# Performance work log

Hardware: AMD Instinct MI355X
Metric: run time of the kernel (lower is better)

The kernel has to match this reference:

```python
import jax, jax.numpy as jnp
import numpy as np
import math

DIM = 256
HEADS = 8
HID = DIM * HEADS


def mish(x):
    return x * jnp.tanh(jax.nn.softplus(x))


def setup_inputs() -> dict:
    key = jax.random.key(0)
    ks = jax.random.split(key, 12)
    b, t, l = 4, 16, 256
    s = 1.0 / math.sqrt(DIM)
    inp = {
        "qkv_x": jax.random.normal(ks[0], (b, t, l, DIM), jnp.float32),
        "t_embed": jax.random.normal(ks[1], (b, t, 1, DIM), jnp.float32),
        "reward_embed": jax.random.normal(ks[2], (b, t, 1, DIM), jnp.float32),
        "Wq": jax.random.normal(ks[3], (DIM, HID), jnp.float32) * s,
        "Wk": jax.random.normal(ks[4], (DIM, HID), jnp.float32) * s,
        "Wv": jax.random.normal(ks[5], (DIM, HID), jnp.float32) * s,
        "Wq_t": jax.random.normal(ks[6], (DIM, HID), jnp.float32) * s,
        "bq_t": jnp.zeros((HID,), jnp.float32),
        "Wk_t": jax.random.normal(ks[7], (DIM, HID), jnp.float32) * s,
        "bk_t": jnp.zeros((HID,), jnp.float32),
        "Wv_t": jax.random.normal(ks[8], (DIM, HID), jnp.float32) * s,
        "bv_t": jnp.zeros((HID,), jnp.float32),
        "Wo": jax.random.normal(ks[9], (HID, DIM), jnp.float32) * (1.0 / math.sqrt(HID)),
        "bo": jnp.zeros((DIM,), jnp.float32),
    }
    return inp


def reference(qkv_x, t_embed, reward_embed, Wq, Wk, Wv, Wq_t, bq_t, Wk_t, bk_t, Wv_t, bv_t, Wo, bo):
    b, t, l, f = qkv_x.shape
    x = qkv_x.reshape(b * t, l, f)                    # (bt, l, f)
    tr = (t_embed + reward_embed).reshape(b * t, 1, f)  # (bt, 1, f)
    m = mish(tr)

    def proj(W, Wt, bt_):
        # bias-add of time-conditioning broadcast over l, split heads
        y = x @ W + (m @ Wt + bt_)                    # (bt, l, H*D)
        return y.reshape(b * t, l, HEADS, DIM).transpose(0, 2, 1, 3)  # (bt, H, l, D)

    q = proj(Wq, Wq_t, bq_t)
    k = proj(Wk, Wk_t, bk_t)
    v = proj(Wv, Wv_t, bv_t)

    scores = jnp.einsum('bhqd,bhkd->bhqk', q, k) / math.sqrt(DIM)
    attn = jax.nn.softmax(scores, axis=-1)
    out = jnp.einsum('bhqk,bhkd->bhqd', attn, v)      # (bt, H, l, D)
    out = out.transpose(0, 2, 1, 3).reshape(b, t, l, HEADS * DIM)
    return out @ Wo + bo
```

## Files before the change

### kernel.cpp

```cpp
#include <hip/hip_runtime.h>
#include <stdint.h>

typedef __bf16 bf16x8 __attribute__((ext_vector_type(8)));
typedef float f32x4 __attribute__((ext_vector_type(4)));
typedef uint32_t u32x4 __attribute__((ext_vector_type(4)));

#define MFMA16(a,b,c) __builtin_amdgcn_mfma_f32_16x16x32_bf16(a,b,c,0,0,0)

#define OFF_XB   0ull
#define OFF_WT   8388608ull
#define OFF_WTT  11534336ull
#define OFF_WOT  14680064ull
#define OFF_MB   15728640ull
#define OFF_BIAS 15761408ull
#define OFF_K    17334272ull
#define OFF_VT   84443136ull
#define WS_NEED  151552000ull
#define OFF_Q    151552000ull
#define WS_NEED2 218660864ull

__device__ __forceinline__ uint16_t f2bf(float f) {
  uint32_t u = __builtin_bit_cast(uint32_t, f);
  return (uint16_t)((u + 0x7fffu + ((u >> 16) & 1u)) >> 16);
}
__device__ __forceinline__ bf16x8 ld16(const uint16_t* p) {
  u32x4 v = *(const u32x4*)p;
  return __builtin_bit_cast(bf16x8, v);
}
__device__ __forceinline__ void gll16(const uint16_t* g, char* l) {
  __builtin_amdgcn_global_load_lds(
      (const __attribute__((address_space(1))) void*)g,
      (__attribute__((address_space(3))) void*)l, 16, 0, 0);
}
__device__ __forceinline__ void bounce_w2(char* slab, int row, int col, uint16_t val) {
  int slot = col >> 3;
  *(uint16_t*)(slab + row * 256 + (((slot ^ (row & 7)) & 15) << 4) + ((col & 7) << 1)) = val;
}
__device__ __forceinline__ bf16x8 bounce_r16(const char* slab, int row, int slot) {
  u32x4 v = *(const u32x4*)(slab + row * 256 + (((slot ^ (row & 7)) & 15) << 4));
  return __builtin_bit_cast(bf16x8, v);
}

__global__ void sentinel_kernel(float* out, float val) {
  out[blockIdx.x * 256 + threadIdx.x] = val;
}
__global__ void init_out(const float* bo, float* out) {
  int i = blockIdx.x * 256 + threadIdx.x;
  out[i] = bo[i & 255];
}

__global__ void mish_kernel(const float* te, const float* re, uint16_t* mb) {
  int i = blockIdx.x * 256 + threadIdx.x;
  float x = te[i] + re[i];
  float sp = log1pf(__expf(x));
  mb[i] = f2bf(x * tanhf(sp));
}

__global__ void convx_kernel(const float* x, uint16_t* xb) {
  int i = blockIdx.x * 256 + threadIdx.x;
  float4 v = ((const float4*)x)[i];
  ushort4 o = make_ushort4(f2bf(v.x), f2bf(v.y), f2bf(v.z), f2bf(v.w));
  ((ushort4*)xb)[i] = o;
}

__global__ void wtrans_kernel(const float* w0, const float* w1, const float* w2,
                              const float* w3, const float* w4, const float* w5,
                              const float* w6, uint16_t* wt, uint16_t* wtt, uint16_t* wot) {
  int z = blockIdx.y;
  const float* src; uint16_t* dst; int C;
  if (z < 3)      { src = (z==0)?w0:((z==1)?w1:w2); dst = wt  + (size_t)z*524288;     C=2048; }
  else if (z < 6) { src = (z==3)?w3:((z==4)?w4:w5); dst = wtt + (size_t)(z-3)*524288; C=2048; }
  else            { src = w6; dst = wot;                                              C=256; }
  int R = (z < 6) ? 256 : 2048;
  __shared__ uint16_t tile[32][33];
  int tc = C >> 5;
  int bR = (blockIdx.x / tc) << 5, bC = (blockIdx.x % tc) << 5;
  int tx = threadIdx.x & 31, ty = threadIdx.x >> 5;
  #pragma unroll
  for (int i = 0; i < 4; i++) {
    int r = bR + ty + i * 8;
    tile[ty + i * 8][tx] = f2bf(src[(size_t)r * C + bC + tx]);
  }
  __syncthreads();
  #pragma unroll
  for (int i = 0; i < 4; i++) {
    int c = bC + ty + i * 8;
    dst[(size_t)c * R + bR + tx] = tile[tx][ty + i * 8];
  }
}

__global__ __launch_bounds__(256, 4)
void bias_gemm(const uint16_t* Mb, const uint16_t* WTT,
               const float* bq, const float* bk, const float* bv, float* biasAll) {
  int bid = blockIdx.x;
  int z = bid >> 4, nbt = bid & 15;
  int n0 = nbt << 7;
  const uint16_t* Bsrc = WTT + (size_t)z * 524288;
  const float* bvec = (z == 0) ? bq : ((z == 1) ? bk : bv);
  float* outp = biasAll + (size_t)z * 131072;
  int tid = threadIdx.x, lane = tid & 63, w = tid >> 6;
  int g = lane >> 4, ln = lane & 15;

  bf16x8 af[8];
  #pragma unroll
  for (int ks = 0; ks < 8; ks++)
    af[ks] = ld16(Mb + (size_t)(w*16 + ln) * 256 + ks*32 + g*8);
  f32x4 acc[8];
  #pragma unroll
  for (int j = 0; j < 8; j++) acc[j] = (f32x4){0.f,0.f,0.f,0.f};
  #pragma unroll
  for (int j = 0; j < 8; j++)
    #pragma unroll
    for (int ks = 0; ks < 8; ks++) {
      bf16x8 bf_ = ld16(Bsrc + (size_t)(n0 + j*16 + ln) * 256 + ks*32 + g*8);
      acc[j] = MFMA16(af[ks], bf_, acc[j]);
    }
  #pragma unroll
  for (int j = 0; j < 8; j++) {
    int colg = n0 + j*16 + ln;
    float bb = bvec[colg];
    #pragma unroll
    for (int r = 0; r < 4; r++)
      outp[(size_t)(w*16 + g*4 + r) * 2048 + colg] = acc[j][r] + bb;
  }
}

__global__ __launch_bounds__(256)
void qkv_gemm3(const uint16_t* Xb, const uint16_t* WT, const float* biasAll,
               uint16_t* Kw, uint16_t* Vt, uint16_t* Qw) {
  __shared__ char stage[32768];
  int nwg = gridDim.x, cpx = nwg >> 3;
  int b0 = blockIdx.x;
  int bid = (b0 & 7) * cpx + (b0 >> 3);
  int z2 = bid >> 11, rem = bid & 2047;
  int widx = (z2 + 1) % 3;
  int mb = rem >> 4, nb = rem & 15;
  int m0 = mb << 7, n0 = nb << 7;
  const uint16_t* Bsrc = WT + (size_t)widx * 524288;
  int bt = m0 >> 8;
  const float* bias = biasAll + (size_t)widx * 131072 + (size_t)bt * 2048;
  int tid = threadIdx.x, lane = tid & 63, w = tid >> 6;
  int g = lane >> 4, ln = lane & 15;
  int wr = w >> 1, wc = w & 1;
  int rw = lane >> 3;
  int sg = (lane & 7) ^ rw;

  f32x4 acc[4][4];
  #pragma unroll
  for (int i = 0; i < 4; i++)
    #pragma unroll
    for (int j = 0; j < 4; j++) acc[i][j] = (f32x4){0.f,0.f,0.f,0.f};

  for (int kt = 0; kt < 4; kt++) {
    int k0 = kt << 6;
    __syncthreads();
    #pragma unroll
    for (int c = 0; c < 4; c++) {
      int chunk = w * 4 + c;
      int row = chunk * 8 + rw;
      gll16(Xb   + (size_t)(m0 + row) * 256 + k0 + sg * 8, stage + chunk * 1024);
      gll16(Bsrc + (size_t)(n0 + row) * 256 + k0 + sg * 8, stage + 16384 + chunk * 1024);
    }
    __syncthreads();
    #pragma unroll
    for (int ks = 0; ks < 2; ks++) {
      bf16x8 a_[4];
      #pragma unroll
      for (int i = 0; i < 4; i++) {
        int R = wr*64 + i*16 + ln;
        u32x4 v = *(const u32x4*)(stage + R*128 + ((((ks<<2)+g) ^ (R & 7)) << 4));
        a_[i] = __builtin_bit_cast(bf16x8, v);
      }
      #pragma unroll
      for (int j = 0; j < 4; j++) {
        int R = wc*64 + j*16 + ln;
        u32x4 v = *(const u32x4*)(stage + 16384 + R*128 + ((((ks<<2)+g) ^ (R & 7)) << 4));
        bf16x8 b_ = __builtin_bit_cast(bf16x8, v);
        #pragma unroll
        for (int i = 0; i < 4; i++) acc[i][j] = MFMA16(a_[i], b_, acc[i][j]);
      }
    }
  }

  __syncthreads();
  char* esl = stage + (w << 13);
  float scale = (z2 == 2) ? 0.0625f : 1.0f;
  int hh = n0 >> 8;
  size_t hb = (size_t)(bt * 8 + hh) << 16;
  int dbase = (n0 & 255) + wc*64;
  int lbase = (m0 & 255) + wr*64;

  if (z2 == 1) {
    #pragma unroll
    for (int j = 0; j < 4; j++) {
      float bb = bias[n0 + wc*64 + j*16 + ln];
      int row = j*16 + ln;
      #pragma unroll
      for (int i = 0; i < 4; i++) {
        int col0 = i*16 + g*4;
        ushort4 pk = make_ushort4(f2bf(acc[i][j][0]+bb), f2bf(acc[i][j][1]+bb),
                                  f2bf(acc[i][j][2]+bb), f2bf(acc[i][j][3]+bb));
        *(ushort4*)(esl + row*128 + ((((col0 >> 3) ^ (row & 7)) & 7) << 4)
                    + ((col0 & 7) << 1)) = pk;
      }
    }
  } else {
    #pragma unroll
    for (int j = 0; j < 4; j++) {
      float bb = bias[n0 + wc*64 + j*16 + ln];
      int slotb = j*2 + (ln >> 3), bcol = (ln & 7) << 1;
      #pragma unroll
      for (int i = 0; i < 4; i++)
        #pragma unroll
        for (int r = 0; r < 4; r++) {
          int row = i*16 + g*4 + r;
          *(uint16_t*)(esl + row*128 + (((slotb ^ (row & 7)) & 7) << 4) + bcol)
              = f2bf((acc[i][j][r] + bb) * scale);
        }
    }
  }
  #pragma unroll
  for (int it = 0; it < 8; it++) {
    int idx = it*64 + lane;
    int row = idx >> 3, ch = idx & 7;
    u32x4 v = *(const u32x4*)(esl + row*128 + (((ch ^ (row & 7)) & 7) << 4));
    if (z2 == 1) {
      *(u32x4*)(Vt + hb + ((size_t)(dbase + row) << 8) + lbase + ch*8) = v;
    } else {
      uint16_t* dst = (z2 == 0) ? Kw : Qw;
      *(u32x4*)(dst + hb + ((size_t)(lbase + row) << 8) + dbase + ch*8) = v;
    }
  }
}

__global__ __launch_bounds__(1024, 2)
void attn_core2(const uint16_t* Qw, const uint16_t* Kw, const uint16_t* Vt, uint16_t* Ob) {
  __shared__ char smem[65536];
  int tid = threadIdx.x, lane = tid & 63, w = tid >> 6;
  int g = lane >> 4, ln = lane & 15;
  int bh = blockIdx.x;
  const size_t kvbase = (size_t)bh << 16;
  int q0l = w * 16;
  char* stage = smem;
  char* slab  = smem + 32768 + (w << 11);

  u32x4 rv[2];
  auto issue_tile = [&](const uint16_t* src) {
    #pragma unroll
    for (int it = 0; it < 2; it++) {
      int c = tid + (it << 10);
      int row = c >> 5, sl = c & 31;
      rv[it] = *(const u32x4*)(src + (size_t)row * 256 + sl * 8);
    }
  };
  auto commit_tile = [&]() {
    #pragma unroll
    for (int it = 0; it < 2; it++) {
      int c = tid + (it << 10);
      int row = c >> 5, sl = c & 31;
      *(u32x4*)(stage + row * 512 + ((sl ^ (row & 7)) << 4)) = rv[it];
    }
  };
  auto frag = [&](int row, int slot) -> bf16x8 {
    u32x4 v = *(const u32x4*)(stage + row * 512 + ((slot ^ (row & 7)) << 4));
    return __builtin_bit_cast(bf16x8, v);
  };

  issue_tile(Kw + kvbase);
  bf16x8 qa[8];
  #pragma unroll
  for (int ks = 0; ks < 8; ks++)
    qa[ks] = ld16(Qw + kvbase + (size_t)(q0l + ln) * 256 + ks*32 + g*8);

  f32x4 S[16];
  #pragma unroll
  for (int f = 0; f < 16; f++) S[f] = (f32x4){0.f,0.f,0.f,0.f};
  #pragma unroll
  for (int t = 0; t < 4; t++) {
    __syncthreads();
    commit_tile();
    __syncthreads();
    if (t < 3) issue_tile(Kw + kvbase + (size_t)((t+1)*64) * 256);
    #pragma unroll
    for (int ks = 0; ks < 8; ks++)
      #pragma unroll
      for (int f2 = 0; f2 < 4; f2++)
        S[t*4+f2] = MFMA16(qa[ks], frag(f2*16 + ln, ks*4 + g), S[t*4+f2]);
  }
  issue_tile(Vt + kvbase);

  #pragma unroll
  for (int r = 0; r < 4; r++) {
    float mx = -3.4e38f;
    #pragma unroll
    for (int f = 0; f < 16; f++) mx = fmaxf(mx, S[f][r]);
    #pragma unroll
    for (int m_ = 1; m_ < 16; m_ <<= 1) mx = fmaxf(mx, __shfl_xor(mx, m_, 64));
    float sum = 0.f;
    #pragma unroll
    for (int f = 0; f < 16; f++) {
      float p = __expf(S[f][r] - mx);
      S[f][r] = p; sum += p;
    }
    #pragma unroll
    for (int m_ = 1; m_ < 16; m_ <<= 1) sum += __shfl_xor(sum, m_, 64);
    float inv = 1.f / sum;
    #pragma unroll
    for (int f = 0; f < 16; f++) S[f][r] *= inv;
  }

  bf16x8 pb[8];
  #pragma unroll
  for (int qtr = 0; qtr < 4; qtr++) {
    #pragma unroll
    for (int f2 = 0; f2 < 4; f2++) {
      int col = f2*16 + ln;
      int slot = col >> 3;
      #pragma unroll
      for (int r = 0; r < 4; r++) {
        int row = g*4 + r;
        *(uint16_t*)(slab + row*128 + (((slot ^ (row & 7)) & 7) << 4) + ((col & 7) << 1))
            = f2bf(S[qtr*4+f2][r]);
      }
    }
    #pragma unroll
    for (int i = 0; i < 2; i++) {
      u32x4 v = *(const u32x4*)(slab + ln*128 + ((((i*4+g) ^ (ln & 7)) & 7) << 4));
      pb[qtr*2+i] = __builtin_bit_cast(bf16x8, v);
    }
  }

  f32x4 O[16];
  #pragma unroll
  for (int df = 0; df < 16; df++) O[df] = (f32x4){0.f,0.f,0.f,0.f};
  #pragma unroll
  for (int t = 0; t < 4; t++) {
    __syncthreads();
    commit_tile();
    __syncthreads();
    if (t < 3) issue_tile(Vt + kvbase + (size_t)((t+1)*64) * 256);
    #pragma unroll
    for (int ks = 0; ks < 8; ks++)
      #pragma unroll
      for (int df2 = 0; df2 < 4; df2++)
        O[t*4+df2] = MFMA16(frag(df2*16 + ln, ks*4 + g), pb[ks], O[t*4+df2]);
  }

  size_t obase = kvbase + (size_t)(q0l + ln) * 256;
  #pragma unroll
  for (int df = 0; df < 16; df++) {
    ushort4 pk = make_ushort4(f2bf(O[df][0]), f2bf(O[df][1]), f2bf(O[df][2]), f2bf(O[df][3]));
    *(ushort4*)(Ob + obase + df*16 + g*4) = pk;
  }
}

__global__ __launch_bounds__(256, 4)
void out_gemm(const uint16_t* Ob, const uint16_t* WoT, const float* bo, float* out) {
  __shared__ char stage[16384];
  int b0 = blockIdx.x;
  int bid = (b0 & 7) * 64 + (b0 >> 3);
  int mt = bid >> 1, nt = bid & 1;
  int m0 = mt << 6, n0 = nt << 7;
  int bt = m0 >> 8;
  int lrow = (m0 & 255);
  int tid = threadIdx.x, lane = tid & 63, w = tid >> 6;
  int g = lane >> 4, ln = lane & 15;

  u32x4 rb[4];
  auto issueW = [&](int kt) {
    #pragma unroll
    for (int it = 0; it < 4; it++) {
      int c = tid + (it << 8);
      int row = c >> 3, sl = c & 7;
      rb[it] = *(const u32x4*)(WoT + (size_t)(n0 + row) * 2048 + kt*64 + sl*8);
    }
  };
  auto aptr = [&](int kt) -> const uint16_t* {
    return Ob + ((size_t)(bt*8 + (kt >> 2)) << 16)
         + (size_t)(lrow + w*16 + ln) * 256 + (kt & 3) * 64;
  };
  issueW(0);
  bf16x8 afc[2];
  { const uint16_t* ab = aptr(0); afc[0] = ld16(ab + g*8); afc[1] = ld16(ab + 32 + g*8); }
  f32x4 acc[8];
  #pragma unroll
  for (int j = 0; j < 8; j++) acc[j] = (f32x4){0.f,0.f,0.f,0.f};

  for (int kt = 0; kt < 32; kt++) {
    __syncthreads();
    #pragma unroll
    for (int it = 0; it < 4; it++) {
      int c = tid + (it << 8);
      int row = c >> 3, sl = c & 7;
      *(u32x4*)(stage + row*128 + (((sl ^ (row & 7)) & 7) << 4)) = rb[it];
    }
    __syncthreads();
    bf16x8 afn[2];
    if (kt < 31) {
      issueW(kt+1);
      const uint16_t* ab = aptr(kt+1);
      afn[0] = ld16(ab + g*8); afn[1] = ld16(ab + 32 + g*8);
    }
    #pragma unroll
    for (int ks = 0; ks < 2; ks++)
      #pragma unroll
      for (int j = 0; j < 8; j++) {
        int row = j*16 + ln;
        u32x4 v = *(const u32x4*)(stage + row*128 + ((((ks*4+g) ^ (row & 7)) & 7) << 4));
        acc[j] = MFMA16(afc[ks], __builtin_bit_cast(bf16x8, v), acc[j]);
      }
    if (kt < 31) { afc[0] = afn[0]; afc[1] = afn[1]; }
  }
  #pragma unroll
  for (int j = 0; j < 8; j++) {
    int col = n0 + j*16 + ln;
    float bb = bo[col];
    #pragma unroll
    for (int r = 0; r < 4; r++)
      out[(size_t)(m0 + w*16 + g*4 + r) * 256 + col] = acc[j][r] + bb;
  }
}

__global__ __launch_bounds__(512, 2)
void attn_v5(const uint16_t* Xb, const uint16_t* WT, const float* Bi,
             const uint16_t* Kw, const uint16_t* Vt, const uint16_t* WoT,
             float* out) {
  __shared__ char smem[65536];
  int tid = threadIdx.x, lane = tid & 63, w = tid >> 6;
  int g = lane >> 4, ln = lane & 15;
  int bid = blockIdx.x;
  int bh = bid >> 1, qh = bid & 1;
  int bt = bh >> 3, h = bh & 7;
  const size_t kvbase = (size_t)bh << 16;
  int q0g = bt * 256 + qh * 128 + w * 16;
  char* stage = smem;
  char* slab  = smem + 32768 + (w << 12);

  u32x4 rv[4];
  auto issue_tile = [&](const uint16_t* src, int rowstride) {
    #pragma unroll
    for (int it = 0; it < 4; it++) {
      int c = tid + (it << 9);
      int row = c >> 5, sl = c & 31;
      rv[it] = *(const u32x4*)(src + (size_t)row * rowstride + sl * 8);
    }
  };
  auto commit_tile = [&]() {
    #pragma unroll
    for (int it = 0; it < 4; it++) {
      int c = tid + (it << 9);
      int row = c >> 5, sl = c & 31;
      *(u32x4*)(stage + row * 512 + ((sl ^ (row & 7)) << 4)) = rv[it];
    }
  };
  auto frag = [&](int row, int slot) -> bf16x8 {
    u32x4 v = *(const u32x4*)(stage + row * 512 + ((slot ^ (row & 7)) << 4));
    return __builtin_bit_cast(bf16x8, v);
  };

  issue_tile(WT + (size_t)(h*256) * 256, 256);
  bf16x8 qx[8];
  #pragma unroll
  for (int ks = 0; ks < 8; ks++)
    qx[ks] = ld16(Xb + (size_t)(q0g + ln) * 256 + ks*32 + g*8);
  f32x4 qacc[16];
  #pragma unroll
  for (int f = 0; f < 16; f++) qacc[f] = (f32x4){0.f,0.f,0.f,0.f};
  #pragma unroll
  for (int t = 0; t < 4; t++) {
    __syncthreads();
    commit_tile();
    __syncthreads();
    if (t < 3) issue_tile(WT + (size_t)(h*256 + (t+1)*64) * 256, 256);
    #pragma unroll
    for (int ks = 0; ks < 8; ks++)
      #pragma unroll
      for (int f2 = 0; f2 < 4; f2++)
        qacc[t*4+f2] = MFMA16(qx[ks], frag(f2*16 + ln, ks*4 + g), qacc[t*4+f2]);
  }
  issue_tile(Kw + kvbase, 256);
  #pragma unroll
  for (int f = 0; f < 16; f++) {
    float bb = Bi[bt*2048 + h*256 + f*16 + ln];
    #pragma unroll
    for (int r = 0; r < 4; r++) qacc[f][r] = (qacc[f][r] + bb) * 0.0625f;
  }
  bf16x8 qa[8];
  #pragma unroll
  for (int dh = 0; dh < 2; dh++) {
    #pragma unroll
    for (int f2 = 0; f2 < 8; f2++) {
      int f = dh*8 + f2;
      #pragma unroll
      for (int r = 0; r < 4; r++)
        bounce_w2(slab, g*4 + r, f2*16 + ln, f2bf(qacc[f][r]));
    }
    #pragma unroll
    for (int ks2 = 0; ks2 < 4; ks2++)
      qa[dh*4 + ks2] = bounce_r16(slab, ln, ks2*4 + g);
  }

  f32x4 S[16];
  #pragma unroll
  for (int f = 0; f < 16; f++) S[f] = (f32x4){0.f,0.f,0.f,0.f};
  #pragma unroll
  for (int t = 0; t < 4; t++) {
    __syncthreads();
    commit_tile();
    __syncthreads();
    if (t < 3) issue_tile(Kw + kvbase + (size_t)((t+1)*64) * 256, 256);
    #pragma unroll
    for (int ks = 0; ks < 8; ks++)
      #pragma unroll
      for (int f2 = 0; f2 < 4; f2++)
        S[t*4+f2] = MFMA16(qa[ks], frag(f2*16 + ln, ks*4 + g), S[t*4+f2]);
  }
  issue_tile(Vt + kvbase, 256);

  #pragma unroll
  for (int r = 0; r < 4; r++) {
    float mx = -3.4e38f;
    #pragma unroll
    for (int f = 0; f < 16; f++) mx = fmaxf(mx, S[f][r]);
    #pragma unroll
    for (int m_ = 1; m_ < 16; m_ <<= 1) mx = fmaxf(mx, __shfl_xor(mx, m_, 64));
    float sum = 0.f;
    #pragma unroll
    for (int f = 0; f < 16; f++) {
      float p = __expf(S[f][r] - mx);
      S[f][r] = p; sum += p;
    }
    #pragma unroll
    for (int m_ = 1; m_ < 16; m_ <<= 1) sum += __shfl_xor(sum, m_, 64);
    float inv = 1.f / sum;
    #pragma unroll
    for (int f = 0; f < 16; f++) S[f][r] *= inv;
  }

  bf16x8 pb[8];
  #pragma unroll
  for (int kh = 0; kh < 2; kh++) {
    #pragma unroll
    for (int f2 = 0; f2 < 8; f2++) {
      int f = kh*8 + f2;
      #pragma unroll
      for (int r = 0; r < 4; r++)
        bounce_w2(slab, g*4 + r, f2*16 + ln, f2bf(S[f][r]));
    }
    #pragma unroll
    for (int ks2 = 0; ks2 < 4; ks2++)
      pb[kh*4 + ks2] = bounce_r16(slab, ln, ks2*4 + g);
  }

  f32x4 O[16];
  #pragma unroll
  for (int df = 0; df < 16; df++) O[df] = (f32x4){0.f,0.f,0.f,0.f};
  #pragma unroll
  for (int t = 0; t < 4; t++) {
    __syncthreads();
    commit_tile();
    __syncthreads();
    if (t < 3) issue_tile(Vt + kvbase + (size_t)((t+1)*64) * 256, 256);
    #pragma unroll
    for (int ks = 0; ks < 8; ks++)
      #pragma unroll
      for (int df2 = 0; df2 < 4; df2++)
        O[t*4+df2] = MFMA16(frag(df2*16 + ln, ks*4 + g), pb[ks], O[t*4+df2]);
  }
  issue_tile(WoT + (size_t)0 * 2048 + h*256, 2048);

  bf16x8 oa[8];
  #pragma unroll
  for (int dh = 0; dh < 2; dh++) {
    #pragma unroll
    for (int df2 = 0; df2 < 8; df2++) {
      int df = dh*8 + df2;
      #pragma unroll
      for (int r = 0; r < 4; r++)
        bounce_w2(slab, ln, df2*16 + g*4 + r, f2bf(O[df][r]));
    }
    #pragma unroll
    for (int ks2 = 0; ks2 < 4; ks2++)
      oa[dh*4 + ks2] = bounce_r16(slab, ln, ks2*4 + g);
  }

  f32x4 oacc[16];
  #pragma unroll
  for (int ef = 0; ef < 16; ef++) oacc[ef] = (f32x4){0.f,0.f,0.f,0.f};
  #pragma unroll
  for (int t = 0; t < 4; t++) {
    __syncthreads();
    commit_tile();
    __syncthreads();
    if (t < 3) issue_tile(WoT + (size_t)((t+1)*64) * 2048 + h*256, 2048);
    #pragma unroll
    for (int ks = 0; ks < 8; ks++)
      #pragma unroll
      for (int ef2 = 0; ef2 < 4; ef2++)
        oacc[t*4+ef2] = MFMA16(oa[ks], frag(ef2*16 + ln, ks*4 + g), oacc[t*4+ef2]);
  }
  #pragma unroll
  for (int ef = 0; ef < 16; ef++)
    #pragma unroll
    for (int r = 0; r < 4; r++)
      atomicAdd(out + (size_t)(q0g + g*4 + r) * 256 + ef*16 + ln, oacc[ef][r]);
}

extern "C" void kernel_launch(void* const* d_in, const int* in_sizes, int n_in,
                              void* d_out, int out_size, void* d_ws, size_t ws_size,
                              hipStream_t stream) {
  float* out = (float*)d_out;
  if (ws_size < WS_NEED) {
    sentinel_kernel<<<16384, 256, 0, stream>>>(out, 1000.0f + (float)(ws_size >> 20));
    return;
  }
  const float* x   = (const float*)d_in[0];
  const float* te  = (const float*)d_in[1];
  const float* re  = (const float*)d_in[2];
  const float* Wq  = (const float*)d_in[3];
  const float* Wk  = (const float*)d_in[4];
  const float* Wv  = (const float*)d_in[5];
  const float* Wqt = (const float*)d_in[6];
  const float* bqt = (const float*)d_in[7];
  const float* Wkt = (const float*)d_in[8];
  const float* bkt = (const float*)d_in[9];
  const float* Wvt = (const float*)d_in[10];
  const float* bvt = (const float*)d_in[11];
  const float* Wo  = (const float*)d_in[12];
  const float* bo  = (const float*)d_in[13];
  char* ws = (char*)d_ws;
  uint16_t* Xb  = (uint16_t*)(ws + OFF_XB);
  uint16_t* WT  = (uint16_t*)(ws + OFF_WT);
  uint16_t* WTT = (uint16_t*)(ws + OFF_WTT);
  uint16_t* WoT = (uint16_t*)(ws + OFF_WOT);
  uint16_t* Mb  = (uint16_t*)(ws + OFF_MB);
  float*    Bi  = (float*)(ws + OFF_BIAS);
  uint16_t* Kw  = (uint16_t*)(ws + OFF_K);
  uint16_t* Vt  = (uint16_t*)(ws + OFF_VT);

  mish_kernel<<<64, 256, 0, stream>>>(te, re, Mb);
  wtrans_kernel<<<dim3(512, 7), 256, 0, stream>>>(Wq, Wk, Wv, Wqt, Wkt, Wvt, Wo, WT, WTT, WoT);
  convx_kernel<<<4096, 256, 0, stream>>>(x, Xb);
  bias_gemm<<<48, 256, 0, stream>>>(Mb, WTT, bqt, bkt, bvt, Bi);

  if (ws_size >= WS_NEED2) {
    uint16_t* Qw = (uint16_t*)(ws + OFF_Q);
    qkv_gemm3<<<6144, 256, 0, stream>>>(Xb, WT, Bi, Kw, Vt, Qw);
    attn_core2<<<512, 1024, 0, stream>>>(Qw, Kw, Vt, Qw);
    out_gemm<<<512, 256, 0, stream>>>(Qw, WoT, bo, out);
  } else {
    qkv_gemm3<<<4096, 256, 0, stream>>>(Xb, WT, Bi, Kw, Vt, Kw);
    init_out<<<16384, 256, 0, stream>>>(bo, out);
    attn_v5<<<1024, 512, 0, stream>>>(Xb, WT, Bi, Kw, Vt, WoT, out);
  }
}
```

Measured before the change: 217.3 us.

## Merge prep kernels into one launch and use direct global-to-LDS loads in attention

The mish, x conversion and weight transpose kernels are folded into a single prep_all launch, with the block index selecting the role. This removes two launch gaps. The attention kernel's K/V staging no longer goes through registers followed by an LDS commit; gll16 copies global memory straight into the swizzled LDS stage. In exchange, the previous overlap, where the next tile's global load was issued during the current tile's MFMAs, is dropped. Each tile load is now exposed between barriers.

```diff
diff --git a/kernel.cpp b/kernel.cpp
--- a/kernel.cpp
+++ b/kernel.cpp
@@ -49,24 +49,28 @@
   out[i] = bo[i & 255];
 }
 
-__global__ void mish_kernel(const float* te, const float* re, uint16_t* mb) {
-  int i = blockIdx.x * 256 + threadIdx.x;
-  float x = te[i] + re[i];
-  float sp = log1pf(__expf(x));
-  mb[i] = f2bf(x * tanhf(sp));
-}
-
-__global__ void convx_kernel(const float* x, uint16_t* xb) {
-  int i = blockIdx.x * 256 + threadIdx.x;
-  float4 v = ((const float4*)x)[i];
-  ushort4 o = make_ushort4(f2bf(v.x), f2bf(v.y), f2bf(v.z), f2bf(v.w));
-  ((ushort4*)xb)[i] = o;
-}
-
-__global__ void wtrans_kernel(const float* w0, const float* w1, const float* w2,
-                              const float* w3, const float* w4, const float* w5,
-                              const float* w6, uint16_t* wt, uint16_t* wtt, uint16_t* wot) {
-  int z = blockIdx.y;
+__global__ void prep_all(const float* te, const float* re, uint16_t* mb,
+                         const float* x, uint16_t* xb,
+                         const float* w0, const float* w1, const float* w2,
+                         const float* w3, const float* w4, const float* w5,
+                         const float* w6, uint16_t* wt, uint16_t* wtt, uint16_t* wot) {
+  int b = blockIdx.x;
+  if (b < 64) {
+    int i = b * 256 + threadIdx.x;
+    float v = te[i] + re[i];
+    float sp = log1pf(__expf(v));
+    mb[i] = f2bf(v * tanhf(sp));
+    return;
+  }
+  if (b < 4160) {
+    int i = (b - 64) * 256 + threadIdx.x;
+    float4 v = ((const float4*)x)[i];
+    ushort4 o = make_ushort4(f2bf(v.x), f2bf(v.y), f2bf(v.z), f2bf(v.w));
+    ((ushort4*)xb)[i] = o;
+    return;
+  }
+  int local = b - 4160;
+  int z = local >> 9, bx = local & 511;
   const float* src; uint16_t* dst; int C;
   if (z < 3)      { src = (z==0)?w0:((z==1)?w1:w2); dst = wt  + (size_t)z*524288;     C=2048; }
   else if (z < 6) { src = (z==3)?w3:((z==4)?w4:w5); dst = wtt + (size_t)(z-3)*524288; C=2048; }
@@ -74,7 +78,7 @@
   int R = (z < 6) ? 256 : 2048;
   __shared__ uint16_t tile[32][33];
   int tc = C >> 5;
-  int bR = (blockIdx.x / tc) << 5, bC = (blockIdx.x % tc) << 5;
+  int bR = (bx / tc) << 5, bC = (bx % tc) << 5;
   int tx = threadIdx.x & 31, ty = threadIdx.x >> 5;
   #pragma unroll
   for (int i = 0; i < 4; i++) {
@@ -234,7 +238,7 @@
 }
 
 __global__ __launch_bounds__(1024, 2)
-void attn_core2(const uint16_t* Qw, const uint16_t* Kw, const uint16_t* Vt, uint16_t* Ob) {
+void attn_core3(const uint16_t* Qw, const uint16_t* Kw, const uint16_t* Vt, uint16_t* Ob) {
   __shared__ char smem[65536];
   int tid = threadIdx.x, lane = tid & 63, w = tid >> 6;
   int g = lane >> 4, ln = lane & 15;
@@ -244,21 +248,14 @@
   char* stage = smem;
   char* slab  = smem + 32768 + (w << 11);
 
-  u32x4 rv[2];
-  auto issue_tile = [&](const uint16_t* src) {
-    #pragma unroll
-    for (int it = 0; it < 2; it++) {
-      int c = tid + (it << 10);
-      int row = c >> 5, sl = c & 31;
-      rv[it] = *(const u32x4*)(src + (size_t)row * 256 + sl * 8);
-    }
-  };
-  auto commit_tile = [&]() {
-    #pragma unroll
-    for (int it = 0; it < 2; it++) {
-      int c = tid + (it << 10);
-      int row = c >> 5, sl = c & 31;
-      *(u32x4*)(stage + row * 512 + ((sl ^ (row & 7)) << 4)) = rv[it];
+  int grow0 = (w << 2) + (lane >> 5);
+  int p = lane & 31;
+  auto gstage = [&](const uint16_t* src) {
+    #pragma unroll
+    for (int c2 = 0; c2 < 2; c2++) {
+      int row = grow0 + c2*2;
+      int sl = p ^ (row & 7);
+      gll16(src + (size_t)row * 256 + sl * 8, stage + (w*2 + c2) * 1024);
     }
   };
   auto frag = [&](int row, int slot) -> bf16x8 {
@@ -266,7 +263,6 @@
     return __builtin_bit_cast(bf16x8, v);
   };
 
-  issue_tile(Kw + kvbase);
   bf16x8 qa[8];
   #pragma unroll
   for (int ks = 0; ks < 8; ks++)
@@ -278,16 +274,14 @@
   #pragma unroll
   for (int t = 0; t < 4; t++) {
     __syncthreads();
-    commit_tile();
-    __syncthreads();
-    if (t < 3) issue_tile(Kw + kvbase + (size_t)((t+1)*64) * 256);
+    gstage(Kw + kvbase + (size_t)(t*64) * 256);
+    __syncthreads();
     #pragma unroll
     for (int ks = 0; ks < 8; ks++)
       #pragma unroll
       for (int f2 = 0; f2 < 4; f2++)
         S[t*4+f2] = MFMA16(qa[ks], frag(f2*16 + ln, ks*4 + g), S[t*4+f2]);
   }
-  issue_tile(Vt + kvbase);
 
   #pragma unroll
   for (int r = 0; r < 4; r++) {
@@ -299,8 +293,8 @@
     float sum = 0.f;
     #pragma unroll
     for (int f = 0; f < 16; f++) {
-      float p = __expf(S[f][r] - mx);
-      S[f][r] = p; sum += p;
+      float pv = __expf(S[f][r] - mx);
+      S[f][r] = pv; sum += pv;
     }
     #pragma unroll
     for (int m_ = 1; m_ < 16; m_ <<= 1) sum += __shfl_xor(sum, m_, 64);
@@ -336,9 +330,8 @@
   #pragma unroll
   for (int t = 0; t < 4; t++) {
     __syncthreads();
-    commit_tile();
-    __syncthreads();
-    if (t < 3) issue_tile(Vt + kvbase + (size_t)((t+1)*64) * 256);
+    gstage(Vt + kvbase + (size_t)(t*64) * 256);
+    __syncthreads();
     #pragma unroll
     for (int ks = 0; ks < 8; ks++)
       #pragma unroll
@@ -638,15 +631,14 @@
   uint16_t* Kw  = (uint16_t*)(ws + OFF_K);
   uint16_t* Vt  = (uint16_t*)(ws + OFF_VT);
 
-  mish_kernel<<<64, 256, 0, stream>>>(te, re, Mb);
-  wtrans_kernel<<<dim3(512, 7), 256, 0, stream>>>(Wq, Wk, Wv, Wqt, Wkt, Wvt, Wo, WT, WTT, WoT);
-  convx_kernel<<<4096, 256, 0, stream>>>(x, Xb);
+  prep_all<<<7744, 256, 0, stream>>>(te, re, Mb, x, Xb,
+                                     Wq, Wk, Wv, Wqt, Wkt, Wvt, Wo, WT, WTT, WoT);
   bias_gemm<<<48, 256, 0, stream>>>(Mb, WTT, bqt, bkt, bvt, Bi);
 
   if (ws_size >= WS_NEED2) {
     uint16_t* Qw = (uint16_t*)(ws + OFF_Q);
     qkv_gemm3<<<6144, 256, 0, stream>>>(Xb, WT, Bi, Kw, Vt, Qw);
-    attn_core2<<<512, 1024, 0, stream>>>(Qw, Kw, Vt, Qw);
+    attn_core3<<<512, 1024, 0, stream>>>(Qw, Kw, Vt, Qw);
     out_gemm<<<512, 256, 0, stream>>>(Qw, WoT, bo, out);
   } else {
     qkv_gemm3<<<4096, 256, 0, stream>>>(Xb, WT, Bi, Kw, Vt, Kw);
```

Result: no change. 216.1 us (-0.6%).

## Fuse prep kernels into one launch and double QKV GEMM M-tile to 256

Applied to the files above, without the earlier changes.

The mish, x-conversion and weight-transpose kernels are merged into a single prep_all launch that dispatches on block index, saving two launches. The QKV projection GEMM now computes a 256x128 tile per workgroup instead of 128x128, reusing each loaded B fragment across two M halves and halving the grid. The cost is more LDS (48KB) and twice the accumulator registers, which may lower occupancy. The epilogue loops over both M halves, reusing the same per-wave staging slab.

```diff
diff --git a/kernel.cpp b/kernel.cpp
--- a/kernel.cpp
+++ b/kernel.cpp
@@ -49,24 +49,28 @@
   out[i] = bo[i & 255];
 }
 
-__global__ void mish_kernel(const float* te, const float* re, uint16_t* mb) {
-  int i = blockIdx.x * 256 + threadIdx.x;
-  float x = te[i] + re[i];
-  float sp = log1pf(__expf(x));
-  mb[i] = f2bf(x * tanhf(sp));
-}
-
-__global__ void convx_kernel(const float* x, uint16_t* xb) {
-  int i = blockIdx.x * 256 + threadIdx.x;
-  float4 v = ((const float4*)x)[i];
-  ushort4 o = make_ushort4(f2bf(v.x), f2bf(v.y), f2bf(v.z), f2bf(v.w));
-  ((ushort4*)xb)[i] = o;
-}
-
-__global__ void wtrans_kernel(const float* w0, const float* w1, const float* w2,
-                              const float* w3, const float* w4, const float* w5,
-                              const float* w6, uint16_t* wt, uint16_t* wtt, uint16_t* wot) {
-  int z = blockIdx.y;
+__global__ void prep_all(const float* te, const float* re, uint16_t* mb,
+                         const float* x, uint16_t* xb,
+                         const float* w0, const float* w1, const float* w2,
+                         const float* w3, const float* w4, const float* w5,
+                         const float* w6, uint16_t* wt, uint16_t* wtt, uint16_t* wot) {
+  int b = blockIdx.x;
+  if (b < 64) {
+    int i = b * 256 + threadIdx.x;
+    float v = te[i] + re[i];
+    float sp = log1pf(__expf(v));
+    mb[i] = f2bf(v * tanhf(sp));
+    return;
+  }
+  if (b < 4160) {
+    int i = (b - 64) * 256 + threadIdx.x;
+    float4 v = ((const float4*)x)[i];
+    ushort4 o = make_ushort4(f2bf(v.x), f2bf(v.y), f2bf(v.z), f2bf(v.w));
+    ((ushort4*)xb)[i] = o;
+    return;
+  }
+  int local = b - 4160;
+  int z = local >> 9, bx = local & 511;
   const float* src; uint16_t* dst; int C;
   if (z < 3)      { src = (z==0)?w0:((z==1)?w1:w2); dst = wt  + (size_t)z*524288;     C=2048; }
   else if (z < 6) { src = (z==3)?w3:((z==4)?w4:w5); dst = wtt + (size_t)(z-3)*524288; C=2048; }
@@ -74,7 +78,7 @@
   int R = (z < 6) ? 256 : 2048;
   __shared__ uint16_t tile[32][33];
   int tc = C >> 5;
-  int bR = (blockIdx.x / tc) << 5, bC = (blockIdx.x % tc) << 5;
+  int bR = (bx / tc) << 5, bC = (bx % tc) << 5;
   int tx = threadIdx.x & 31, ty = threadIdx.x >> 5;
   #pragma unroll
   for (int i = 0; i < 4; i++) {
@@ -126,18 +130,18 @@
 }
 
 __global__ __launch_bounds__(256)
-void qkv_gemm3(const uint16_t* Xb, const uint16_t* WT, const float* biasAll,
+void qkv_gemm5(const uint16_t* Xb, const uint16_t* WT, const float* biasAll,
                uint16_t* Kw, uint16_t* Vt, uint16_t* Qw) {
-  __shared__ char stage[32768];
+  __shared__ char stage[49152];
   int nwg = gridDim.x, cpx = nwg >> 3;
   int b0 = blockIdx.x;
   int bid = (b0 & 7) * cpx + (b0 >> 3);
-  int z2 = bid >> 11, rem = bid & 2047;
+  int z2 = bid >> 10, rem = bid & 1023;
   int widx = (z2 + 1) % 3;
-  int mb = rem >> 4, nb = rem & 15;
-  int m0 = mb << 7, n0 = nb << 7;
+  int mt = rem >> 4, nb = rem & 15;
+  int m0 = mt << 8, n0 = nb << 7;
   const uint16_t* Bsrc = WT + (size_t)widx * 524288;
-  int bt = m0 >> 8;
+  int bt = mt;
   const float* bias = biasAll + (size_t)widx * 131072 + (size_t)bt * 2048;
   int tid = threadIdx.x, lane = tid & 63, w = tid >> 6;
   int g = lane >> 4, ln = lane & 15;
@@ -145,39 +149,53 @@
   int rw = lane >> 3;
   int sg = (lane & 7) ^ rw;
 
-  f32x4 acc[4][4];
-  #pragma unroll
-  for (int i = 0; i < 4; i++)
-    #pragma unroll
-    for (int j = 0; j < 4; j++) acc[i][j] = (f32x4){0.f,0.f,0.f,0.f};
+  f32x4 acc[2][4][4];
+  #pragma unroll
+  for (int mh = 0; mh < 2; mh++)
+    #pragma unroll
+    for (int i = 0; i < 4; i++)
+      #pragma unroll
+      for (int j = 0; j < 4; j++) acc[mh][i][j] = (f32x4){0.f,0.f,0.f,0.f};
 
   for (int kt = 0; kt < 4; kt++) {
     int k0 = kt << 6;
     __syncthreads();
+    #pragma unroll
+    for (int c = 0; c < 8; c++) {
+      int chunk = w * 8 + c;
+      int row = chunk * 8 + rw;
+      gll16(Xb + (size_t)(m0 + row) * 256 + k0 + sg * 8, stage + chunk * 1024);
+    }
     #pragma unroll
     for (int c = 0; c < 4; c++) {
       int chunk = w * 4 + c;
       int row = chunk * 8 + rw;
-      gll16(Xb   + (size_t)(m0 + row) * 256 + k0 + sg * 8, stage + chunk * 1024);
-      gll16(Bsrc + (size_t)(n0 + row) * 256 + k0 + sg * 8, stage + 16384 + chunk * 1024);
+      gll16(Bsrc + (size_t)(n0 + row) * 256 + k0 + sg * 8, stage + 32768 + chunk * 1024);
     }
     __syncthreads();
     #pragma unroll
     for (int ks = 0; ks < 2; ks++) {
-      bf16x8 a_[4];
-      #pragma unroll
-      for (int i = 0; i < 4; i++) {
-        int R = wr*64 + i*16 + ln;
-        u32x4 v = *(const u32x4*)(stage + R*128 + ((((ks<<2)+g) ^ (R & 7)) << 4));
-        a_[i] = __builtin_bit_cast(bf16x8, v);
-      }
+      bf16x8 fb[4];
       #pragma unroll
       for (int j = 0; j < 4; j++) {
         int R = wc*64 + j*16 + ln;
-        u32x4 v = *(const u32x4*)(stage + 16384 + R*128 + ((((ks<<2)+g) ^ (R & 7)) << 4));
-        bf16x8 b_ = __builtin_bit_cast(bf16x8, v);
+        u32x4 v = *(const u32x4*)(stage + 32768 + R*128 + ((((ks<<1)*2+g) ^ (R & 7)) << 4));
+        fb[j] = __builtin_bit_cast(bf16x8, v);
+      }
+      #pragma unroll
+      for (int mh = 0; mh < 2; mh++) {
+        bf16x8 fa[4];
         #pragma unroll
-        for (int i = 0; i < 4; i++) acc[i][j] = MFMA16(a_[i], b_, acc[i][j]);
+        for (int i = 0; i < 4; i++) {
+          int R = mh*128 + wr*64 + i*16 + ln;
+          u32x4 v = *(const u32x4*)(stage + R*128 + ((((ks<<2)+g) ^ (R & 7)) << 4));
+          fa[i] = __builtin_bit_cast(bf16x8, v);
+        }
+        #pragma unroll
+        for (int j = 0; j < 4; j++)
+          #pragma unroll
+          for (int i = 0; i < 4; i++)
+            acc[mh][i][j] = MFMA16(fa[i], fb[j], acc[mh][i][j]);
       }
     }
   }
@@ -188,47 +206,50 @@
   int hh = n0 >> 8;
   size_t hb = (size_t)(bt * 8 + hh) << 16;
   int dbase = (n0 & 255) + wc*64;
-  int lbase = (m0 & 255) + wr*64;
-
-  if (z2 == 1) {
-    #pragma unroll
-    for (int j = 0; j < 4; j++) {
-      float bb = bias[n0 + wc*64 + j*16 + ln];
-      int row = j*16 + ln;
-      #pragma unroll
-      for (int i = 0; i < 4; i++) {
-        int col0 = i*16 + g*4;
-        ushort4 pk = make_ushort4(f2bf(acc[i][j][0]+bb), f2bf(acc[i][j][1]+bb),
-                                  f2bf(acc[i][j][2]+bb), f2bf(acc[i][j][3]+bb));
-        *(ushort4*)(esl + row*128 + ((((col0 >> 3) ^ (row & 7)) & 7) << 4)
-                    + ((col0 & 7) << 1)) = pk;
+
+  #pragma unroll
+  for (int mh = 0; mh < 2; mh++) {
+    int lbase = mh*128 + wr*64;
+    if (z2 == 1) {
+      #pragma unroll
+      for (int j = 0; j < 4; j++) {
+        float bb = bias[n0 + wc*64 + j*16 + ln];
+        int row = j*16 + ln;
+        #pragma unroll
+        for (int i = 0; i < 4; i++) {
+          int col0 = i*16 + g*4;
+          ushort4 pk = make_ushort4(f2bf(acc[mh][i][j][0]+bb), f2bf(acc[mh][i][j][1]+bb),
+                                    f2bf(acc[mh][i][j][2]+bb), f2bf(acc[mh][i][j][3]+bb));
+          *(ushort4*)(esl + row*128 + ((((col0 >> 3) ^ (row & 7)) & 7) << 4)
+                      + ((col0 & 7) << 1)) = pk;
+        }
       }
-    }
-  } else {
-    #pragma unroll
-    for (int j = 0; j < 4; j++) {
-      float bb = bias[n0 + wc*64 + j*16 + ln];
-      int slotb = j*2 + (ln >> 3), bcol = (ln & 7) << 1;
-      #pragma unroll
-      for (int i = 0; i < 4; i++)
+    } else {
+      #pragma unroll
+      for (int j = 0; j < 4; j++) {
+        float bb = bias[n0 + wc*64 + j*16 + ln];
+        int slotb = j*2 + (ln >> 3), bcol = (ln & 7) << 1;
         #pragma unroll
-        for (int r = 0; r < 4; r++) {
-          int row = i*16 + g*4 + r;
-          *(uint16_t*)(esl + row*128 + (((slotb ^ (row & 7)) & 7) << 4) + bcol)
-              = f2bf((acc[i][j][r] + bb) * scale);
-        }
-    }
-  }
-  #pragma unroll
-  for (int it = 0; it < 8; it++) {
-    int idx = it*64 + lane;
-    int row = idx >> 3, ch = idx & 7;
-    u32x4 v = *(const u32x4*)(esl + row*128 + (((ch ^ (row & 7)) & 7) << 4));
-    if (z2 == 1) {
-      *(u32x4*)(Vt + hb + ((size_t)(dbase + row) << 8) + lbase + ch*8) = v;
-    } else {
-      uint16_t* dst = (z2 == 0) ? Kw : Qw;
-      *(u32x4*)(dst + hb + ((size_t)(lbase + row) << 8) + dbase + ch*8) = v;
+        for (int i = 0; i < 4; i++)
+          #pragma unroll
+          for (int r = 0; r < 4; r++) {
+            int row = i*16 + g*4 + r;
+            *(uint16_t*)(esl + row*128 + (((slotb ^ (row & 7)) & 7) << 4) + bcol)
+                = f2bf((acc[mh][i][j][r] + bb) * scale);
+          }
+      }
+    }
+    #pragma unroll
+    for (int it = 0; it < 8; it++) {
+      int idx = it*64 + lane;
+      int row = idx >> 3, ch = idx & 7;
+      u32x4 v = *(const u32x4*)(esl + row*128 + (((ch ^ (row & 7)) & 7) << 4));
+      if (z2 == 1) {
+        *(u32x4*)(Vt + hb + ((size_t)(dbase + row) << 8) + lbase + ch*8) = v;
+      } else {
+        uint16_t* dst = (z2 == 0) ? Kw : Qw;
+        *(u32x4*)(dst + hb + ((size_t)(lbase + row) << 8) + dbase + ch*8) = v;
+      }
     }
   }
 }
@@ -638,18 +659,17 @@
   uint16_t* Kw  = (uint16_t*)(ws + OFF_K);
   uint16_t* Vt  = (uint16_t*)(ws + OFF_VT);
 
-  mish_kernel<<<64, 256, 0, stream>>>(te, re, Mb);
-  wtrans_kernel<<<dim3(512, 7), 256, 0, stream>>>(Wq, Wk, Wv, Wqt, Wkt, Wvt, Wo, WT, WTT, WoT);
-  convx_kernel<<<4096, 256, 0, stream>>>(x, Xb);
+  prep_all<<<7744, 256, 0, stream>>>(te, re, Mb, x, Xb,
+                                     Wq, Wk, Wv, Wqt, Wkt, Wvt, Wo, WT, WTT, WoT);
   bias_gemm<<<48, 256, 0, stream>>>(Mb, WTT, bqt, bkt, bvt, Bi);
 
   if (ws_size >= WS_NEED2) {
     uint16_t* Qw = (uint16_t*)(ws + OFF_Q);
-    qkv_gemm3<<<6144, 256, 0, stream>>>(Xb, WT, Bi, Kw, Vt, Qw);
+    qkv_gemm5<<<3072, 256, 0, stream>>>(Xb, WT, Bi, Kw, Vt, Qw);
     attn_core2<<<512, 1024, 0, stream>>>(Qw, Kw, Vt, Qw);
     out_gemm<<<512, 256, 0, stream>>>(Qw, WoT, bo, out);
   } else {
-    qkv_gemm3<<<4096, 256, 0, stream>>>(Xb, WT, Bi, Kw, Vt, Kw);
+    qkv_gemm5<<<2048, 256, 0, stream>>>(Xb, WT, Bi, Kw, Vt, Kw);
     init_out<<<16384, 256, 0, stream>>>(bo, out);
     attn_v5<<<1024, 512, 0, stream>>>(Xb, WT, Bi, Kw, Vt, WoT, out);
   }
```

Result: slower. 260.8 us (+20.0%).
